# Kernel tuning notes

Hardware: AMD Instinct MI355X
Metric: run time of the kernel (lower is better)

## Reference

```python
import jax, jax.numpy as jnp
import numpy as np

B, S, D, F, E = 8, 2048, 768, 3072, 8


def setup_inputs() -> dict:
    key = jax.random.key(0)
    k1, k2, k3, k4 = jax.random.split(key, 4)
    return {
        "hidden_states": jax.random.normal(k1, (B, S, D), dtype=jnp.float32),
        "router_w": jax.random.normal(k2, (D, E), dtype=jnp.float32) * 0.02,
        "w_in": jax.random.normal(k3, (E, D, F), dtype=jnp.float32) * 0.02,
        "w_out": jax.random.normal(k4, (E, F, D), dtype=jnp.float32) * 0.02,
    }


def reference(hidden_states, router_w, w_in, w_out):
    b, s, d = hidden_states.shape
    x = hidden_states.reshape(-1, d)                    # [T, D] tokens
    router_logits = x @ router_w                        # [T, E]
    router_probs_full = jax.nn.softmax(router_logits, axis=-1)
    expert_index = jnp.argmax(router_probs_full, axis=-1)          # top-1 routing
    onehot = jax.nn.one_hot(expert_index, E, dtype=x.dtype)        # [T, E] router_mask
    top_prob = jnp.max(router_probs_full, axis=-1, keepdims=True)  # [T, 1] router_probs

    # Per-expert FFN (relu MLP); every token is processed by exactly one expert,
    # expert outputs overwrite the token (gather/scatter combine in the original).
    y = jnp.zeros_like(x)
    for e in range(E):  # fixed small expert count; weights structurally distinct
        h = jax.nn.relu(x @ w_in[e]) @ w_out[e]
        y = y + onehot[:, e:e + 1] * h

    out = (top_prob * y).reshape(b, s, d)
    return out, router_logits, expert_index
```

## Files before the change

kernel.cpp:

```cpp
#include <hip/hip_runtime.h>
#include <hip/hip_bf16.h>

constexpr int T  = 16384;
constexpr int Dh = 768;
constexpr int Fh = 3072;
constexpr int Eh = 8;
constexpr int MAXTILES = 136;

typedef unsigned short ushort_t;
typedef __attribute__((ext_vector_type(8))) short  bf16x8;
typedef __attribute__((ext_vector_type(4))) float  f32x4;

static __device__ __forceinline__ ushort_t f2bf(float f) {
    unsigned u = __builtin_bit_cast(unsigned, f);
    u += 0x7FFFu + ((u >> 16) & 1u);
    return (ushort_t)(u >> 16);
}

__global__ void init_counts(int* counts) {
    if (threadIdx.x < Eh) counts[threadIdx.x] = 0;
}

__global__ __launch_bounds__(1024) void router_kernel(
    const float* __restrict__ x, const float* __restrict__ rw,
    float* __restrict__ logits_out, float* __restrict__ eidx_out,
    float* __restrict__ topp, int* __restrict__ counts, int* __restrict__ perm) {

    __shared__ float rwT[Eh][Dh];
    __shared__ int   sAmax[16];
    __shared__ int   sBase[Eh];

    int tid = threadIdx.x;
    for (int i = tid; i < Dh * Eh; i += 1024) {
        int d = i >> 3, e = i & 7;
        rwT[e][d] = rw[i];
    }
    __syncthreads();

    int wave = tid >> 6, lane = tid & 63;
    int t = blockIdx.x * 16 + wave;
    const float* xr = x + (size_t)t * Dh;

    double acc[Eh];
#pragma unroll
    for (int e = 0; e < Eh; ++e) acc[e] = 0.0;

#pragma unroll
    for (int j = 0; j < Dh / 256; ++j) {
        int d = lane * 4 + j * 256;
        const float4 xv = *(const float4*)(xr + d);
#pragma unroll
        for (int e = 0; e < Eh; ++e) {
            const float4 w = *(const float4*)&rwT[e][d];
            acc[e] += (double)xv.x * (double)w.x + (double)xv.y * (double)w.y
                    + (double)xv.z * (double)w.z + (double)xv.w * (double)w.w;
        }
    }
#pragma unroll
    for (int off = 32; off > 0; off >>= 1) {
#pragma unroll
        for (int e = 0; e < Eh; ++e) acc[e] += __shfl_xor(acc[e], off, 64);
    }

    int amax = 0;
    if (lane == 0) {
        float l32[Eh];
        float m = -3.4e38f;
#pragma unroll
        for (int e = 0; e < Eh; ++e) l32[e] = (float)acc[e];
#pragma unroll
        for (int e = 0; e < Eh; ++e) {
            if (l32[e] > m) { m = l32[e]; amax = e; }
        }
        float s = 0.f;
#pragma unroll
        for (int e = 0; e < Eh; ++e) s += expf(l32[e] - m);
#pragma unroll
        for (int e = 0; e < Eh; ++e) logits_out[(size_t)t * Eh + e] = l32[e];
        eidx_out[t] = (float)amax;
        topp[t]     = 1.0f / s;
        sAmax[wave] = amax;
    }
    __syncthreads();

    if (tid < Eh) {
        int c = 0;
#pragma unroll
        for (int w = 0; w < 16; ++w) c += (sAmax[w] == tid);
        sBase[tid] = (c > 0) ? atomicAdd(&counts[tid], c) : 0;
    }
    __syncthreads();

    if (lane == 0) {
        int prior = 0;
        for (int w = 0; w < wave; ++w) prior += (sAmax[w] == amax);
        perm[amax * T + sBase[amax] + prior] = t;
    }
}

__global__ void scan_counts(const int* counts, int* offsets,
                            int* tE, int* tGoff, int* tSlot0, int* tRows, int* nT) {
    if (threadIdx.x == 0) {
        int off = 0, n = 0;
        for (int e = 0; e < Eh; ++e) {
            offsets[e] = off;
            int c = counts[e];
            for (int t0 = 0; t0 < c; t0 += 128) {
                tE[n] = e; tGoff[n] = off + t0; tSlot0[n] = t0;
                tRows[n] = (c - t0 < 128) ? (c - t0) : 128;
                ++n;
            }
            off += c;
        }
        offsets[Eh] = off;
        nT[0] = n;
    }
}

__global__ void gather_cast_x(const float* __restrict__ x, const int* __restrict__ offsets,
                              const int* __restrict__ perm, ushort_t* __restrict__ Xg) {
    __shared__ int soff[Eh + 1];
    if (threadIdx.x < Eh + 1) soff[threadIdx.x] = offsets[threadIdx.x];
    __syncthreads();
    int q  = blockIdx.x * 256 + threadIdx.x;
    int g  = q / (Dh / 4);
    int cq = (q - g * (Dh / 4)) * 4;
    int e = 0;
#pragma unroll
    for (int i = 1; i < Eh; ++i) e += (g >= soff[i]);
    int tok = perm[e * T + (g - soff[e])];
    const float4 v = *(const float4*)(x + (size_t)tok * Dh + cq);
    ushort4 o;
    o.x = f2bf(v.x); o.y = f2bf(v.y); o.z = f2bf(v.z); o.w = f2bf(v.w);
    *(ushort4*)(Xg + (size_t)g * Dh + cq) = o;
}

__global__ void transpose_cvt(const float* __restrict__ src, ushort_t* __restrict__ dst,
                              int R, int C) {
    __shared__ ushort_t tile[32][33];
    int tx = threadIdx.x, ty = threadIdx.y;
    size_t base = (size_t)blockIdx.z * (size_t)R * (size_t)C;
    int c0 = blockIdx.x * 32, r0 = blockIdx.y * 32;
#pragma unroll
    for (int j = 0; j < 4; ++j) {
        int r = ty + j * 8;
        tile[r][tx] = f2bf(src[base + (size_t)(r0 + r) * C + c0 + tx]);
    }
    __syncthreads();
    int idx = ty * 32 + tx;
#pragma unroll
    for (int j = 0; j < 2; ++j) {
        int lin = idx + j * 256;
        int c  = lin >> 4;
        int rp = (lin & 15) * 2;
        ushort2 o = { tile[rp][c], tile[rp + 1][c] };
        *(ushort2*)(dst + base + (size_t)(c0 + c) * R + r0 + rp) = o;
    }
}

template<int KTOT, int NTOT, int MODE>
__global__ __launch_bounds__(256) void moe_gemm(
    const ushort_t* __restrict__ Aall, const ushort_t* __restrict__ Ball,
    const int* __restrict__ tE, const int* __restrict__ tGoff,
    const int* __restrict__ tSlot0, const int* __restrict__ tRows,
    const int* __restrict__ nT,
    const int* __restrict__ perm, const float* __restrict__ topp,
    void* __restrict__ Cout)
{
    int i = blockIdx.x;
    if (i >= nT[0]) return;
    int e     = tE[i];
    int goff  = tGoff[i];
    int slot0 = tSlot0[i];
    int rows  = tRows[i];
    int n0    = blockIdx.y * 128;

    const ushort_t* Ap = Aall + (size_t)goff * KTOT;
    const ushort_t* Bp = Ball + (size_t)e * KTOT * NTOT + (size_t)n0 * KTOT;

    __shared__ ushort_t As[128 * 64];
    __shared__ ushort_t Bs[128 * 64];
    __shared__ int   tokLds[128];
    __shared__ float probLds[128];

    int tid = threadIdx.x, lane = tid & 63, wave = tid >> 6;

    if (MODE == 1 && tid < 128) {
        int tok = (tid < rows) ? perm[e * T + slot0 + tid] : 0;
        tokLds[tid]  = tok;
        probLds[tid] = (tid < rows) ? topp[tok] : 0.f;
    }

    f32x4 acc[4][4];
    const f32x4 zero = {0.f, 0.f, 0.f, 0.f};
#pragma unroll
    for (int mi = 0; mi < 4; ++mi)
#pragma unroll
        for (int ni = 0; ni < 4; ++ni) acc[mi][ni] = zero;

    int lrow  = lane >> 3;
    int gsrc8 = ((lane & 7) ^ lrow) * 8;
    int wm    = (wave >> 1) * 64;
    int wn    = (wave & 1) * 64;
    int lm    = lane & 15;
    int lm7   = lm & 7;
    int gq    = lane >> 4;

    for (int k0 = 0; k0 < KTOT; k0 += 64) {
#pragma unroll
        for (int it = 0; it < 4; ++it) {
            int rb  = wave * 4 + it;
            int row = rb * 8 + lrow;
            const ushort_t* ga = Ap + (size_t)row * KTOT + k0 + gsrc8;
            const ushort_t* gb = Bp + (size_t)row * KTOT + k0 + gsrc8;
            __builtin_amdgcn_global_load_lds(
                (const __attribute__((address_space(1))) unsigned int*)ga,
                (__attribute__((address_space(3))) unsigned int*)&As[rb * 512], 16, 0, 0);
            __builtin_amdgcn_global_load_lds(
                (const __attribute__((address_space(1))) unsigned int*)gb,
                (__attribute__((address_space(3))) unsigned int*)&Bs[rb * 512], 16, 0, 0);
        }
        __syncthreads();
#pragma unroll
        for (int kc = 0; kc < 64; kc += 32) {
            int cbase = gq + (kc >> 3);
            bf16x8 af[4], bb[4];
#pragma unroll
            for (int mi = 0; mi < 4; ++mi) {
                int row = wm + mi * 16 + lm;
                af[mi] = *(const bf16x8*)&As[row * 64 + ((cbase ^ lm7) * 8)];
            }
#pragma unroll
            for (int ni = 0; ni < 4; ++ni) {
                int row = wn + ni * 16 + lm;
                bb[ni] = *(const bf16x8*)&Bs[row * 64 + ((cbase ^ lm7) * 8)];
            }
#pragma unroll
            for (int mi = 0; mi < 4; ++mi)
#pragma unroll
                for (int ni = 0; ni < 4; ++ni)
                    acc[mi][ni] = __builtin_amdgcn_mfma_f32_16x16x32_bf16(
                        af[mi], bb[ni], acc[mi][ni], 0, 0, 0);
        }
        __syncthreads();
    }

    int cr = (lane >> 4) * 4;
    int cc = lane & 15;
#pragma unroll
    for (int mi = 0; mi < 4; ++mi) {
#pragma unroll
        for (int r = 0; r < 4; ++r) {
            int m = wm + mi * 16 + cr + r;
            if (m < rows) {
                if (MODE == 0) {
                    ushort_t* hp = (ushort_t*)Cout + (size_t)(goff + m) * NTOT + n0 + wn + cc;
#pragma unroll
                    for (int ni = 0; ni < 4; ++ni) {
                        float v = acc[mi][ni][r];
                        hp[ni * 16] = f2bf(v > 0.f ? v : 0.f);
                    }
                } else {
                    int tok = tokLds[m];
                    float p = probLds[m];
                    float* op = (float*)Cout + (size_t)tok * NTOT + n0 + wn + cc;
#pragma unroll
                    for (int ni = 0; ni < 4; ++ni) op[ni * 16] = acc[mi][ni][r] * p;
                }
            }
        }
    }
}

constexpr size_t OFF_COUNTS  = 0;
constexpr size_t OFF_OFFSETS = 256;
constexpr size_t OFF_TILES   = 512;
constexpr size_t OFF_TOPP    = OFF_TILES + 4 * 144 * 5 + 64;
constexpr size_t OFF_PERM    = OFF_TOPP + (size_t)T * 4;
constexpr size_t OFF_XG      = (OFF_PERM + (size_t)Eh * T * 4 + 255) & ~(size_t)255;
constexpr size_t OFF_H       = (OFF_XG + (size_t)(T + 128) * Dh * 2 + 255) & ~(size_t)255;
constexpr size_t OFF_WIN     = (OFF_H + (size_t)(T + 128) * Fh * 2 + 255) & ~(size_t)255;
constexpr size_t OFF_WOUT    = (OFF_WIN + (size_t)Eh * Dh * Fh * 2 + 255) & ~(size_t)255;

extern "C" void kernel_launch(void* const* d_in, const int* in_sizes, int n_in,
                              void* d_out, int out_size, void* d_ws, size_t ws_size,
                              hipStream_t stream) {
    const float* x    = (const float*)d_in[0];
    const float* rw   = (const float*)d_in[1];
    const float* w_in = (const float*)d_in[2];
    const float* w_out= (const float*)d_in[3];

    float* out    = (float*)d_out;
    float* logits = out + (size_t)T * Dh;
    float* eidx   = logits + (size_t)T * Eh;

    char* ws = (char*)d_ws;
    int*      counts  = (int*)(ws + OFF_COUNTS);
    int*      offsets = (int*)(ws + OFF_OFFSETS);
    int*      tE      = (int*)(ws + OFF_TILES);
    int*      tGoff   = tE + 144;
    int*      tSlot0  = tGoff + 144;
    int*      tRows   = tSlot0 + 144;
    int*      nT      = tRows + 144;
    float*    topp    = (float*)(ws + OFF_TOPP);
    int*      perm    = (int*)(ws + OFF_PERM);
    ushort_t* Xg      = (ushort_t*)(ws + OFF_XG);
    ushort_t* h       = (ushort_t*)(ws + OFF_H);
    ushort_t* WinT    = (ushort_t*)(ws + OFF_WIN);
    ushort_t* WoutT   = (ushort_t*)(ws + OFF_WOUT);

    init_counts<<<1, 64, 0, stream>>>(counts);
    router_kernel<<<T / 16, 1024, 0, stream>>>(x, rw, logits, eidx, topp, counts, perm);
    scan_counts<<<1, 64, 0, stream>>>(counts, offsets, tE, tGoff, tSlot0, tRows, nT);
    gather_cast_x<<<(T * (Dh / 4)) / 256, 256, 0, stream>>>(x, offsets, perm, Xg);
    transpose_cvt<<<dim3(Fh / 32, Dh / 32, Eh), dim3(32, 8), 0, stream>>>(w_in, WinT, Dh, Fh);
    transpose_cvt<<<dim3(Dh / 32, Fh / 32, Eh), dim3(32, 8), 0, stream>>>(w_out, WoutT, Fh, Dh);
    moe_gemm<Dh, Fh, 0><<<dim3(MAXTILES, Fh / 128), 256, 0, stream>>>(
        Xg, WinT, tE, tGoff, tSlot0, tRows, nT, perm, topp, (void*)h);
    moe_gemm<Fh, Dh, 1><<<dim3(MAXTILES, Dh / 128), 256, 0, stream>>>(
        h, WoutT, tE, tGoff, tSlot0, tRows, nT, perm, topp, (void*)out);
}
```

Baseline: 554.0 us.

## Remap MoE GEMM blocks to XCDs for L2 locality and vectorize weight transpose

After: 564.9 us. About the same (+2.0%).

```diff
diff --git a/kernel.cpp b/kernel.cpp
--- a/kernel.cpp
+++ b/kernel.cpp
@@ -137,28 +137,26 @@
 
 __global__ void transpose_cvt(const float* __restrict__ src, ushort_t* __restrict__ dst,
                               int R, int C) {
-    __shared__ ushort_t tile[32][33];
+    __shared__ ushort_t tile[32][36];
     int tx = threadIdx.x, ty = threadIdx.y;
     size_t base = (size_t)blockIdx.z * (size_t)R * (size_t)C;
     int c0 = blockIdx.x * 32, r0 = blockIdx.y * 32;
-#pragma unroll
-    for (int j = 0; j < 4; ++j) {
-        int r = ty + j * 8;
-        tile[r][tx] = f2bf(src[base + (size_t)(r0 + r) * C + c0 + tx]);
-    }
-    __syncthreads();
-    int idx = ty * 32 + tx;
-#pragma unroll
-    for (int j = 0; j < 2; ++j) {
-        int lin = idx + j * 256;
-        int c  = lin >> 4;
-        int rp = (lin & 15) * 2;
-        ushort2 o = { tile[rp][c], tile[rp + 1][c] };
-        *(ushort2*)(dst + base + (size_t)(c0 + c) * R + r0 + rp) = o;
-    }
-}
-
-template<int KTOT, int NTOT, int MODE>
+
+    const float4 v = *(const float4*)(src + base + (size_t)(r0 + ty) * C + c0 + tx * 4);
+    ushort4 o;
+    o.x = f2bf(v.x); o.y = f2bf(v.y); o.z = f2bf(v.z); o.w = f2bf(v.w);
+    *(ushort4*)&tile[ty][tx * 4] = o;
+    __syncthreads();
+
+    int tid = ty * 8 + tx;
+    int c  = tid >> 3;
+    int rq = (tid & 7) * 4;
+    ushort4 w;
+    w.x = tile[rq][c]; w.y = tile[rq + 1][c]; w.z = tile[rq + 2][c]; w.w = tile[rq + 3][c];
+    *(ushort4*)(dst + base + (size_t)(c0 + c) * R + r0 + rq) = w;
+}
+
+template<int KTOT, int NTOT, int MODE, int COLOC>
 __global__ __launch_bounds__(256) void moe_gemm(
     const ushort_t* __restrict__ Aall, const ushort_t* __restrict__ Ball,
     const int* __restrict__ tE, const int* __restrict__ tGoff,
@@ -167,13 +165,19 @@
     const int* __restrict__ perm, const float* __restrict__ topp,
     void* __restrict__ Cout)
 {
-    int i = blockIdx.x;
-    if (i >= nT[0]) return;
-    int e     = tE[i];
-    int goff  = tGoff[i];
-    int slot0 = tSlot0[i];
-    int rows  = tRows[i];
-    int n0    = blockIdx.y * 128;
+    constexpr int NT128 = NTOT / 128;
+    int id = blockIdx.x;
+    int xcd = id & 7, slot = id >> 3;
+    int mt, nt;
+    if (COLOC == 0) { mt = slot % MAXTILES; nt = xcd + 8 * (slot / MAXTILES); }
+    else            { nt = slot % NT128;    mt = (slot / NT128) * 8 + xcd; }
+    if (mt >= nT[0]) return;
+
+    int e     = tE[mt];
+    int goff  = tGoff[mt];
+    int slot0 = tSlot0[mt];
+    int rows  = tRows[mt];
+    int n0    = nt * 128;
 
     const ushort_t* Ap = Aall + (size_t)goff * KTOT;
     const ushort_t* Bp = Ball + (size_t)e * KTOT * NTOT + (size_t)n0 * KTOT;
@@ -313,10 +317,10 @@
     router_kernel<<<T / 16, 1024, 0, stream>>>(x, rw, logits, eidx, topp, counts, perm);
     scan_counts<<<1, 64, 0, stream>>>(counts, offsets, tE, tGoff, tSlot0, tRows, nT);
     gather_cast_x<<<(T * (Dh / 4)) / 256, 256, 0, stream>>>(x, offsets, perm, Xg);
-    transpose_cvt<<<dim3(Fh / 32, Dh / 32, Eh), dim3(32, 8), 0, stream>>>(w_in, WinT, Dh, Fh);
-    transpose_cvt<<<dim3(Dh / 32, Fh / 32, Eh), dim3(32, 8), 0, stream>>>(w_out, WoutT, Fh, Dh);
-    moe_gemm<Dh, Fh, 0><<<dim3(MAXTILES, Fh / 128), 256, 0, stream>>>(
+    transpose_cvt<<<dim3(Fh / 32, Dh / 32, Eh), dim3(8, 32), 0, stream>>>(w_in, WinT, Dh, Fh);
+    transpose_cvt<<<dim3(Dh / 32, Fh / 32, Eh), dim3(8, 32), 0, stream>>>(w_out, WoutT, Fh, Dh);
+    moe_gemm<Dh, Fh, 0, 0><<<8 * (Fh / 128 / 8) * MAXTILES, 256, 0, stream>>>(
         Xg, WinT, tE, tGoff, tSlot0, tRows, nT, perm, topp, (void*)h);
-    moe_gemm<Fh, Dh, 1><<<dim3(MAXTILES, Dh / 128), 256, 0, stream>>>(
+    moe_gemm<Fh, Dh, 1, 1><<<8 * (Dh / 128) * (MAXTILES / 8), 256, 0, stream>>>(
         h, WoutT, tE, tGoff, tSlot0, tRows, nT, perm, topp, (void*)out);
 }
```
